# Optimization experiments

Measured on AMD Instinct MI355X. Metric: run time of the kernel, lower is better.

The kernel has to match this reference:

```python
import jax, jax.numpy as jnp
import numpy as np

D = 640          # feature dim (x_dim)
C = 64           # number of classes
N = 1024         # support samples (16 shots/class)
Q = 2048         # query samples
REG = 0.3        # reg_param


def setup_inputs() -> dict:
    key = jax.random.key(0)
    k0, k1, k2, k3, k4 = jax.random.split(key, 5)
    X = jax.random.normal(k0, (N, D), jnp.float32)
    y = (jnp.arange(N) % C).astype(jnp.int32)          # every class populated
    Xq = jax.random.normal(k1, (Q, D), jnp.float32)
    # learnable prior parameters (perturbed from the torch init so grads are nontrivial)
    m = 0.02 * jax.random.normal(k2, (1, D), jnp.float32)
    kappa = jnp.array([0.1], jnp.float32)
    nu = jnp.array([float(D)], jnp.float32)
    triu_diag = 1.0 + 0.05 * jax.random.normal(k3, (D,), jnp.float32)
    triu_lower = jnp.eye(D, dtype=jnp.float32) + 0.05 * jax.random.normal(k4, (D, D), jnp.float32)
    return {"X": X, "y": y, "Xq": Xq, "m": m, "kappa": kappa, "nu": nu,
            "triu_diag": triu_diag, "triu_lower": triu_lower}


def reference(X, y, Xq, m, kappa, nu, triu_diag, triu_lower):
    # strictly-lower-triangular mask: triu(ones, 1).T
    mask = jnp.triu(jnp.ones((D, D), X.dtype), 1).T
    L = jnp.diag(jnp.abs(triu_diag)) + triu_lower * mask          # Cholesky-like factor
    kappa_ = jnp.abs(kappa[0]) + 1e-6
    nu_ = jnp.maximum(nu[0], D - 1 + 1e-6)

    onehot = jax.nn.one_hot(y, C, dtype=X.dtype)                   # [N, C]
    Nc = onehot.sum(0)                                             # [C]
    mean_c = (onehot.T @ X) / Nc[:, None]                          # [C, D]
    # MAP posterior mean per class
    w = Nc / (kappa_ + Nc)
    mu = (1.0 - w)[:, None] * m + w[:, None] * mean_c              # [C, D]

    # per-class second moment: S_c = sum_{y=c} x x^T (segmented X^T X)
    Xc = onehot.T[:, :, None] * X[None, :, :]                      # [C, N, D]
    S = jnp.einsum('cnd,ne->cde', Xc, X)                           # [C, D, D]

    LLt = L @ L.T
    mm = m.T @ m                                                   # [D, D]
    mu_outer = jnp.einsum('cd,ce->cde', mu, mu)
    sigma = (LLt[None] + S + kappa_ * mm[None]
             - (kappa_ + Nc)[:, None, None] * mu_outer)
    sigma = sigma / (nu_ + Nc + D + 2)[:, None, None]
    sigma_inv = jnp.linalg.inv(sigma)
    sigma_inv = (1.0 - REG) * sigma_inv + REG * jnp.eye(D, dtype=X.dtype)

    # batched Mahalanobis quadratic form: -(x - mu_c)^T Sinv_c (x - mu_c)
    diff = Xq[:, None, :] - mu[None, :, :]                         # [Q, C, D]
    dist = jnp.einsum('qcd,cde,qce->qc', diff, sigma_inv, diff)
    return -dist
```

## Files before the change

kernel.cpp:

```cpp
#include <hip/hip_runtime.h>
#include <hip/hip_bf16.h>


#define D 640
#define C 64
#define NSUP 1024
#define Q 2048
#define KMAX 16
#define R18 18
#define VROWS (C * R18)
#define YROWS 3137
#define YPAD 3200
#define NEXT 704
#define LP 40

typedef __attribute__((ext_vector_type(8))) short bf16x8;
typedef __attribute__((ext_vector_type(4))) float floatx4;

__device__ __forceinline__ unsigned short f2bf(float x) {
    unsigned int u = __float_as_uint(x);
    unsigned int r = u + 0x7FFFu + ((u >> 16) & 1u);
    return (unsigned short)(r >> 16);
}

__device__ __forceinline__ void pack4(const float* vv, unsigned short* hp, unsigned short* lp) {
#pragma unroll
    for (int i = 0; i < 4; ++i) {
        unsigned short hb = f2bf(vv[i]);
        float hf = __uint_as_float((unsigned int)hb << 16);
        hp[i] = hb;
        lp[i] = f2bf(vv[i] - hf);
    }
}

__device__ __forceinline__ void rownorm_body(const float* __restrict__ A, int ld,
                                             float* __restrict__ out, int gw, int lane) {
    const float* row = A + (size_t)gw * ld;
    float s = 0.f;
    for (int d = lane; d < D; d += 64) { float v = row[d]; s += v * v; }
#pragma unroll
    for (int off = 32; off; off >>= 1) s += __shfl_xor(s, off);
    if (lane == 0) out[gw] = s;
}

#define BZCH (640 * 640 / 8)
#define AZCH (63 * 640 / 8)
__global__ void k_setup(const int* __restrict__ y, const float* __restrict__ kappa,
                        const float* __restrict__ nu, const float* __restrict__ diag,
                        int* __restrict__ cnt, int* __restrict__ idx,
                        float* __restrict__ sc, float* __restrict__ rd,
                        int* __restrict__ rowmap,
                        unsigned short* __restrict__ Ah, unsigned short* __restrict__ Al,
                        unsigned short* __restrict__ Bh, unsigned short* __restrict__ Bl) {
    int tid = threadIdx.x;
    if (blockIdx.x > 0) {
        int id = (blockIdx.x - 1) * 256 + tid;
        const uint4 z = {0u, 0u, 0u, 0u};
        if (id < BZCH) ((uint4*)Bh)[id] = z;
        else if (id < 2 * BZCH) ((uint4*)Bl)[id - BZCH] = z;
        else if (id < 2 * BZCH + AZCH) ((uint4*)(Ah + (size_t)YROWS * D))[id - 2 * BZCH] = z;
        else if (id < 2 * BZCH + 2 * AZCH) ((uint4*)(Al + (size_t)YROWS * D))[id - 2 * BZCH - AZCH] = z;
        return;
    }
    __shared__ int lc[C];
    if (tid < C) lc[tid] = 0;
    __syncthreads();
    for (int n = tid; n < NSUP; n += 256) {
        int c = y[n];
        int k = atomicAdd(&lc[c], 1);
        if (k < KMAX) idx[c * KMAX + k] = n;
    }
    __syncthreads();
    for (int d = tid; d < D; d += 256) rd[d] = 1.0f / fabsf(diag[d]);
    if (tid < C) {
        int n = lc[tid]; if (n > KMAX) n = KMAX;
        cnt[tid] = n;
        float kap = fabsf(kappa[0]) + 1e-6f;
        float nuv = fmaxf(nu[0], (float)(D - 1) + 1e-6f);
        float Ncf = (float)n;
        sc[64 + tid]  = Ncf / (kap + Ncf);
        sc[128 + tid] = nuv + Ncf + (float)(D + 2);
        sc[192 + tid] = -1.0f / (kap + Ncf);
        if (tid == 0) { sc[0] = kap; sc[1] = nuv; }
    }
    __syncthreads();
    for (int i = tid; i < VROWS; i += 256) {
        int c = i / R18, j = i - c * R18;
        int nc = lc[c] < KMAX ? lc[c] : KMAX;
        int rm;
        if (j == 0) rm = Q + NSUP;
        else if (j <= KMAX) rm = (j - 1 < nc) ? Q + idx[c * KMAX + j - 1] : -1;
        else rm = Q + NSUP + 1 + c;
        rowmap[i] = rm;
    }
}

__global__ __launch_bounds__(256) void k_dinv_mu(
        const float* __restrict__ tlow, const float* __restrict__ rd,
        float* __restrict__ Linv,
        const float* __restrict__ X, const float* __restrict__ m,
        const int* __restrict__ cnt, const int* __restrict__ idx,
        const float* __restrict__ sc, float* __restrict__ mu,
        const float* __restrict__ Xq,
        unsigned short* __restrict__ Ah, unsigned short* __restrict__ Al,
        unsigned short* __restrict__ Bh, unsigned short* __restrict__ Bl,
        float* __restrict__ a0) {
    __shared__ float Lst[128 * 128];
    int tid = threadIdx.x;
    int bid = blockIdx.x;
    if (bid < 160) {
        int b = bid >> 5;
        int j = ((bid & 31) << 2) + (tid >> 6);
        int lane = tid & 63;
        int bB = b * 128;
        {
            float4 tv[16];
            float rv[16];
#pragma unroll
            for (int u = 0; u < 16; ++u) {
                int e = tid + u * 256;
                int c4 = (e & 31) * 4, r = e >> 5;
                tv[u] = *(const float4*)(tlow + (size_t)(bB + r) * D + bB + c4);
                rv[u] = rd[bB + r];
            }
#pragma unroll
            for (int u = 0; u < 16; ++u) {
                int e = tid + u * 256;
                int c4 = (e & 31) * 4, r = e >> 5;
                float vv[4] = {tv[u].x, tv[u].y, tv[u].z, tv[u].w};
#pragma unroll
                for (int t = 0; t < 4; ++t) {
                    int c = c4 + t;
                    float v;
                    if (r == c) v = 1.0f;
                    else if (r > c) v = rv[u] * vv[t];
                    else v = 0.f;
                    Lst[c * 128 + (r ^ (c & 63))] = v;
                }
            }
        }
        __syncthreads();
        float rd0 = rd[bB + lane], rd1 = rd[bB + 64 + lane];
        float acc0 = 0.f, acc1 = 0.f, zz0 = 0.f, zz1 = 0.f;
        for (int i = j; i < 128; ++i) {
            int ri = i >> 6, il = i & 63;
            float av = (ri == 0) ? acc0 : acc1;
            float ai = __shfl(av, il);
            float zi = (i == j) ? __shfl((ri == 0) ? rd0 : rd1, il) : -ai;
            int sw = i & 63;
            float l0 = Lst[i * 128 + (lane ^ sw)];
            float l1 = Lst[i * 128 + 64 + (lane ^ sw)];
            if (lane > i) acc0 += l0 * zi;
            if (64 + lane > i) acc1 += l1 * zi;
            if (lane == i) zz0 = zi;
            if (64 + lane == i) zz1 = zi;
        }
        Linv[(size_t)(bB + lane) * D + bB + j] = zz0;
        Linv[(size_t)(bB + 64 + lane) * D + bB + j] = zz1;
        unsigned short h0 = f2bf(zz0);
        float hf0 = __uint_as_float((unsigned int)h0 << 16);
        Bh[(size_t)(bB + lane) * D + bB + j] = h0;
        Bl[(size_t)(bB + lane) * D + bB + j] = f2bf(zz0 - hf0);
        unsigned short h1 = f2bf(zz1);
        float hf1 = __uint_as_float((unsigned int)h1 << 16);
        Bh[(size_t)(bB + 64 + lane) * D + bB + j] = h1;
        Bl[(size_t)(bB + 64 + lane) * D + bB + j] = f2bf(zz1 - hf1);
    } else if (bid < 320) {
        int u = (bid - 160) * 2 + (tid >> 7);
        int c = u / 5, by = u - c * 5;
        int d = by * 128 + (tid & 127);
        int n = cnt[c];
        float s = 0.f;
        for (int k = 0; k < n; ++k) s += X[(size_t)idx[c * KMAX + k] * D + d];
        float w = sc[64 + c];
        float mean = (n > 0) ? s / (float)n : 0.f;
        float val = (1.f - w) * m[d] + w * mean;
        mu[(size_t)c * D + d] = val;
        unsigned short hb = f2bf(val);
        float hf = __uint_as_float((unsigned int)hb << 16);
        unsigned short lb = f2bf(val - hf);
        Ah[(size_t)(Q + NSUP + 1 + c) * D + d] = hb;
        Al[(size_t)(Q + NSUP + 1 + c) * D + d] = lb;
        Bh[(size_t)(D + c) * D + d] = hb;
        Bl[(size_t)(D + c) * D + d] = lb;
    } else if (bid < 2240) {
        int gid = (bid - 320) * 256 + tid;
        int row = gid / 160, c = (gid - row * 160) * 4;
        float4 v = (row < Q) ? *(const float4*)(Xq + (size_t)row * D + c)
                             : *(const float4*)(X + (size_t)(row - Q) * D + c);
        float vv[4] = {v.x, v.y, v.z, v.w};
        ushort4 h, l;
        pack4(vv, (unsigned short*)&h, (unsigned short*)&l);
        *(ushort4*)(Ah + (size_t)row * D + c) = h;
        *(ushort4*)(Al + (size_t)row * D + c) = l;
    } else if (bid == 2240) {
        if (tid < 160) {
            int c = tid * 4;
            float4 v = *(const float4*)(m + c);
            float vv[4] = {v.x, v.y, v.z, v.w};
            ushort4 h, l;
            pack4(vv, (unsigned short*)&h, (unsigned short*)&l);
            *(ushort4*)(Ah + (size_t)(Q + NSUP) * D + c) = h;
            *(ushort4*)(Al + (size_t)(Q + NSUP) * D + c) = l;
        }
    } else {
        int gw = ((bid - 2241) * 256 + tid) >> 6;
        rownorm_body(Xq, D, a0, gw, tid & 63);
    }
}

__global__ void k_lhat(const float* __restrict__ tlow, const float* __restrict__ Linv,
                       float* __restrict__ Lhat) {
    const int bi_tab[10] = {1, 2, 2, 3, 3, 3, 4, 4, 4, 4};
    const int bk_tab[10] = {0, 0, 1, 0, 1, 2, 0, 1, 2, 3};
    int p = blockIdx.y;
    int bi = bi_tab[p], bk = bk_tab[p];
    int tid = threadIdx.x;
    int c = tid & 127;
    int r = (blockIdx.x << 1) + (tid >> 7);
    const float* drow = Linv + (size_t)(bi * 128 + r) * D + bi * 128;
    const float* lcol = tlow + (size_t)(bi * 128) * D + bk * 128 + c;
    float s = 0.f;
#pragma unroll 4
    for (int t = 0; t < 128; ++t) s += drow[t] * lcol[(size_t)t * D];
    Lhat[(size_t)(bi * 128 + r) * D + bk * 128 + c] = s;
}

template<int B>
__device__ __forceinline__ void linv_chain(const float* __restrict__ Lhat,
                                           float* __restrict__ Linv,
                                           unsigned short* __restrict__ Bh,
                                           unsigned short* __restrict__ Bl,
                                           float S[4][128][20],
                                           int cB, int tid) {
    const int ty = tid >> 2, tx = tid & 3;
    const int r0 = 2 * ty;
    float acc[4 - B][2][4];
#pragma unroll
    for (int a = 0; a < 4 - B; ++a)
#pragma unroll
        for (int rr = 0; rr < 2; ++rr)
#pragma unroll
            for (int cc = 0; cc < 4; ++cc) acc[a][rr][cc] = 0.f;
#pragma unroll
    for (int js = 0; js < 4 - B; ++js) {
        const int j = B + js;
        for (int k0 = 0; k0 < 128; k0 += 8) {
            float svf[8][4];
#pragma unroll
            for (int u = 0; u < 8; ++u) {
                float4 s4 = *(const float4*)&S[js][k0 + u][tx * 4];
                svf[u][0] = s4.x; svf[u][1] = s4.y; svf[u][2] = s4.z; svf[u][3] = s4.w;
            }
#pragma unroll
            for (int a = js; a < 4 - B; ++a) {
                const int i = B + 1 + a;
                const float* p0 = Lhat + (size_t)(i * 128 + r0) * D + j * 128 + k0;
                const float* p1 = p0 + D;
                float4 a00 = *(const float4*)(p0);
                float4 a01 = *(const float4*)(p0 + 4);
                float4 a10 = *(const float4*)(p1);
                float4 a11 = *(const float4*)(p1 + 4);
                float ar0[8] = {a00.x, a00.y, a00.z, a00.w, a01.x, a01.y, a01.z, a01.w};
                float ar1[8] = {a10.x, a10.y, a10.z, a10.w, a11.x, a11.y, a11.z, a11.w};
#pragma unroll
                for (int u = 0; u < 8; ++u) {
#pragma unroll
                    for (int cc = 0; cc < 4; ++cc) {
                        acc[a][0][cc] += ar0[u] * svf[u][cc];
                        acc[a][1][cc] += ar1[u] * svf[u][cc];
                    }
                }
            }
        }
        {
            const int i = j + 1;
#pragma unroll
            for (int rr = 0; rr < 2; ++rr) {
                const int r = r0 + rr;
                float vv[4];
#pragma unroll
                for (int cc = 0; cc < 4; ++cc) vv[cc] = -acc[js][rr][cc];
                float4 v = {vv[0], vv[1], vv[2], vv[3]};
                if (js + 1 < 4 - B) *(float4*)&S[js + 1][r][tx * 4] = v;
                *(float4*)(Linv + (size_t)(i * 128 + r) * D + cB + tx * 4) = v;
                ushort4 hh, ll;
                pack4(vv, (unsigned short*)&hh, (unsigned short*)&ll);
                *(ushort4*)(Bh + (size_t)(i * 128 + r) * D + cB + tx * 4) = hh;
                *(ushort4*)(Bl + (size_t)(i * 128 + r) * D + cB + tx * 4) = ll;
            }
        }
        if (js + 1 < 4 - B) __syncthreads();
    }
}

__global__ __launch_bounds__(256) void k_linv_fill(const float* __restrict__ Lhat,
                                                   float* __restrict__ Linv,
                                                   unsigned short* __restrict__ Bh,
                                                   unsigned short* __restrict__ Bl) {
    __shared__ __align__(16) float S[4][128][20];
    int tid = threadIdx.x;
    int b = blockIdx.x >> 3, strip = blockIdx.x & 7;
    int bB = b * 128, cB = bB + strip * 16;
    {
        int r = tid >> 1, c0 = (tid & 1) * 8;
        const float* src = Linv + (size_t)(bB + r) * D + cB + c0;
        *(float4*)&S[0][r][c0]     = *(const float4*)(src);
        *(float4*)&S[0][r][c0 + 4] = *(const float4*)(src + 4);
    }
    __syncthreads();
    if (b == 0)      linv_chain<0>(Lhat, Linv, Bh, Bl, S, cB, tid);
    else if (b == 1) linv_chain<1>(Lhat, Linv, Bh, Bl, S, cB, tid);
    else if (b == 2) linv_chain<2>(Lhat, Linv, Bh, Bl, S, cB, tid);
    else             linv_chain<3>(Lhat, Linv, Bh, Bl, S, cB, tid);
}

__global__ __launch_bounds__(256) void k_mfma_nt(
        const unsigned short* __restrict__ Ah, const unsigned short* __restrict__ Al,
        const unsigned short* __restrict__ Bh, const unsigned short* __restrict__ Bl,
        float* __restrict__ Out, int M, int N, int ldo,
        unsigned short* __restrict__ Th, unsigned short* __restrict__ Tl) {
    __shared__ __align__(16) unsigned short SB[2][4][64 * LP];
    int tid = threadIdx.x;
    int rowBase = blockIdx.y * 64, colBase = blockIdx.x * 64;
    int r = tid >> 2, e = (tid & 3) << 3;
    int gr = rowBase + r;
    int gc = colBase + r;
    bool aok = (gr < M), bok = (gc < N);
    int w = tid >> 6, lane = tid & 63, q = lane >> 4, lr = lane & 15;
    int aoff = (16 * w + lr) * LP + q * 8;
    int wr = r * LP + e;
    const uint4 z4 = {0u, 0u, 0u, 0u};
    floatx4 acc[4] = {{0.f, 0.f, 0.f, 0.f}, {0.f, 0.f, 0.f, 0.f},
                      {0.f, 0.f, 0.f, 0.f}, {0.f, 0.f, 0.f, 0.f}};
    uint4 vah, val, vbh, vbl;
#define LOADK(kk) { \
        vah = aok ? *(const uint4*)(Ah + (size_t)gr * D + (kk) + e) : z4; \
        val = aok ? *(const uint4*)(Al + (size_t)gr * D + (kk) + e) : z4; \
        vbh = bok ? *(const uint4*)(Bh + (size_t)gc * D + (kk) + e) : z4; \
        vbl = bok ? *(const uint4*)(Bl + (size_t)gc * D + (kk) + e) : z4; }
    LOADK(0);
    for (int step = 0; step < D / 32; ++step) {
        int cur = step & 1;
        *(uint4*)(&SB[cur][0][wr]) = vah;
        *(uint4*)(&SB[cur][1][wr]) = val;
        *(uint4*)(&SB[cur][2][wr]) = vbh;
        *(uint4*)(&SB[cur][3][wr]) = vbl;
        if (step + 1 < D / 32) LOADK((step + 1) * 32);
        __syncthreads();
        bf16x8 ah = *(const bf16x8*)(&SB[cur][0][aoff]);
        bf16x8 al = *(const bf16x8*)(&SB[cur][1][aoff]);
#pragma unroll
        for (int tt = 0; tt < 4; ++tt) {
            int boff = (16 * tt + lr) * LP + q * 8;
            bf16x8 bh = *(const bf16x8*)(&SB[cur][2][boff]);
            bf16x8 bl = *(const bf16x8*)(&SB[cur][3][boff]);
            acc[tt] = __builtin_amdgcn_mfma_f32_16x16x32_bf16(ah, bh, acc[tt], 0, 0, 0);
            acc[tt] = __builtin_amdgcn_mfma_f32_16x16x32_bf16(ah, bl, acc[tt], 0, 0, 0);
            acc[tt] = __builtin_amdgcn_mfma_f32_16x16x32_bf16(al, bh, acc[tt], 0, 0, 0);
        }
    }
#undef LOADK
#pragma unroll
    for (int tt = 0; tt < 4; ++tt) {
        int gc2 = colBase + 16 * tt + lr;
#pragma unroll
        for (int rg = 0; rg < 4; ++rg) {
            int gr2 = rowBase + 16 * w + q * 4 + rg;
            if (gr2 < M && gc2 < N) {
                float v = acc[tt][rg];
                Out[(size_t)gr2 * ldo + gc2] = v;
                if (Th && gc2 < D) {
                    unsigned short hb = f2bf(v);
                    float hf = __uint_as_float((unsigned int)hb << 16);
                    Th[(size_t)gr2 * D + gc2] = hb;
                    Tl[(size_t)gr2 * D + gc2] = f2bf(v - hf);
                }
            }
        }
    }
}

__global__ __launch_bounds__(256) void k_gv(
        const unsigned short* __restrict__ Th, const unsigned short* __restrict__ Tl,
        const int* __restrict__ rowmap, float* __restrict__ G,
        const float* __restrict__ Yt, const float* __restrict__ mu,
        const float* __restrict__ sc, float* __restrict__ at,
        float* __restrict__ h, float* __restrict__ btil,
        float* __restrict__ b0, float* __restrict__ kinv) {
    __shared__ __align__(16) char smem[40960];
    int bid = blockIdx.x, tid = threadIdx.x;
    if (bid < 64) {
        float (*aug)[40] = (float(*)[40])smem;
        int* rmv = (int*)(smem + 2880);
        int c = bid;
        if (tid < R18) rmv[tid] = rowmap[c * R18 + tid];
        for (int i2 = tid; i2 < R18 * R18; i2 += 256)
            aug[i2 / R18][R18 + i2 % R18] = (i2 / R18 == i2 % R18) ? 1.f : 0.f;
        __syncthreads();
        if (tid < 171) {
            int i = 0, rem = tid;
            while (rem >= R18 - i) { rem -= R18 - i; ++i; }
            int j = i + rem;
            int rmi = rmv[i], rmj = rmv[j];
            float s = 0.f;
            if (rmi >= 0 && rmj >= 0) {
                const float* ri = Yt + (size_t)rmi * NEXT;
                const float* rj = Yt + (size_t)rmj * NEXT;
                float s0 = 0.f, s1 = 0.f, s2 = 0.f, s3 = 0.f;
#pragma unroll 4
                for (int d = 0; d < D; d += 4) {
                    float4 a = *(const float4*)(ri + d);
                    float4 bb = *(const float4*)(rj + d);
                    s0 += a.x * bb.x; s1 += a.y * bb.y;
                    s2 += a.z * bb.z; s3 += a.w * bb.w;
                }
                s = (s0 + s1) + (s2 + s3);
            }
            aug[i][j] = s;
            if (i != j) aug[j][i] = s;
        }
        __syncthreads();
        int w = tid >> 6, lane = tid & 63;
        if (w == 1) {
            const float* mc = mu + (size_t)c * D;
            float s = 0.f;
            for (int d = lane; d < D; d += 64) { float v = mc[d]; s += v * v; }
#pragma unroll
            for (int off = 32; off; off >>= 1) s += __shfl_xor(s, off);
            if (lane == 0) b0[c] = s;
        }
        if (w == 0) {
            if (lane < R18) h[c * R18 + lane] = aug[lane][R18 - 1];
            if (lane == 0) btil[c] = aug[R18 - 1][R18 - 1];
            volatile float (*va)[40] = (volatile float (*)[40])aug;
            if (lane == 0) va[0][0] += 1.0f / sc[0];
            else if (lane <= KMAX) va[lane][lane] += 1.0f;
            else if (lane == R18 - 1) va[R18 - 1][R18 - 1] += sc[192 + c];
            __threadfence_block();
            for (int p = 0; p < R18; ++p) {
                float v = (lane >= p && lane < R18) ? fabsf(va[lane][p]) : -1.f;
                int bi = lane;
#pragma unroll
                for (int off = 32; off; off >>= 1) {
                    float ov = __shfl_xor(v, off);
                    int oi = __shfl_xor(bi, off);
                    if (ov > v || (ov == v && oi < bi)) { v = ov; bi = oi; }
                }
                float pv = va[bi][p];
                if (lane < 2 * R18) {
                    float rp = va[bi][lane];
                    if (bi != p) va[bi][lane] = va[p][lane];
                    va[p][lane] = rp / pv;
                }
                __threadfence_block();
                float f  = (lane < R18) ? va[lane][p] : 0.f;
                float pr = (lane < 2 * R18) ? va[p][lane] : 0.f;
#pragma unroll
                for (int it = 0; it < 11; ++it) {
                    int e = lane + it * 64;
                    int r2 = e / 36, cc = e - r2 * 36;
                    float fr = __shfl(f, r2 < R18 ? r2 : 0);
                    float pc = __shfl(pr, cc);
                    if (e < R18 * 2 * R18 && r2 != p) va[r2][cc] -= fr * pc;
                }
                __threadfence_block();
            }
            for (int e = lane; e < R18 * R18; e += 64)
                kinv[(size_t)c * R18 * R18 + e] = va[e / R18][R18 + e % R18];
        }
    } else if (bid < 640) {
        unsigned short (*SB)[4][64 * LP] = (unsigned short (*)[4][64 * LP])smem;
        int gb = bid - 64;
        int rowBase = (gb / 18) * 64, colBase = (gb % 18) * 64;
        int r = tid >> 2, e = (tid & 3) << 3;
        int gr = rowBase + r;
        int gc = colBase + r;
        int br = rowmap[gc];
        int w = tid >> 6, lane = tid & 63, q = lane >> 4, lr = lane & 15;
        int aoff = (16 * w + lr) * LP + q * 8;
        int wr = r * LP + e;
        const uint4 z4 = {0u, 0u, 0u, 0u};
        floatx4 acc[4] = {{0.f, 0.f, 0.f, 0.f}, {0.f, 0.f, 0.f, 0.f},
                          {0.f, 0.f, 0.f, 0.f}, {0.f, 0.f, 0.f, 0.f}};
        uint4 vah, val, vbh, vbl;
#define LOADG(kk) { \
            vah = *(const uint4*)(Th + (size_t)gr * D + (kk) + e); \
            val = *(const uint4*)(Tl + (size_t)gr * D + (kk) + e); \
            vbh = (br >= 0) ? *(const uint4*)(Th + (size_t)br * D + (kk) + e) : z4; \
            vbl = (br >= 0) ? *(const uint4*)(Tl + (size_t)br * D + (kk) + e) : z4; }
        LOADG(0);
        for (int step = 0; step < D / 32; ++step) {
            int cur = step & 1;
            *(uint4*)(&SB[cur][0][wr]) = vah;
            *(uint4*)(&SB[cur][1][wr]) = val;
            *(uint4*)(&SB[cur][2][wr]) = vbh;
            *(uint4*)(&SB[cur][3][wr]) = vbl;
            if (step + 1 < D / 32) LOADG((step + 1) * 32);
            __syncthreads();
            bf16x8 ah = *(const bf16x8*)(&SB[cur][0][aoff]);
            bf16x8 al = *(const bf16x8*)(&SB[cur][1][aoff]);
#pragma unroll
            for (int tt = 0; tt < 4; ++tt) {
                int boff = (16 * tt + lr) * LP + q * 8;
                bf16x8 bh = *(const bf16x8*)(&SB[cur][2][boff]);
                bf16x8 bl = *(const bf16x8*)(&SB[cur][3][boff]);
                acc[tt] = __builtin_amdgcn_mfma_f32_16x16x32_bf16(ah, bh, acc[tt], 0, 0, 0);
                acc[tt] = __builtin_amdgcn_mfma_f32_16x16x32_bf16(ah, bl, acc[tt], 0, 0, 0);
                acc[tt] = __builtin_amdgcn_mfma_f32_16x16x32_bf16(al, bh, acc[tt], 0, 0, 0);
            }
        }
#undef LOADG
#pragma unroll
        for (int tt = 0; tt < 4; ++tt) {
            int gc2 = colBase + 16 * tt + lr;
#pragma unroll
            for (int rg = 0; rg < 4; ++rg) {
                int gr2 = rowBase + 16 * w + q * 4 + rg;
                G[(size_t)gr2 * VROWS + gc2] = acc[tt][rg];
            }
        }
    } else {
        int gw = ((bid - 640) * 256 + tid) >> 6;
        rownorm_body(Yt, NEXT, at, gw, tid & 63);
    }
}

__global__ void k_epi(const float* __restrict__ G, const float* __restrict__ Yt,
                      const float* __restrict__ at, const float* __restrict__ a0,
                      const float* __restrict__ h, const float* __restrict__ btil,
                      const float* __restrict__ b0, const float* __restrict__ kinv,
                      const float* __restrict__ sc, float* __restrict__ out) {
    __shared__ float lk[R18 * R18], lh[R18];
    __shared__ float ldn, lbt, lb0;
    int c = blockIdx.x, tid = threadIdx.x;
    for (int i = tid; i < R18 * R18; i += 256) lk[i] = kinv[(size_t)c * R18 * R18 + i];
    if (tid < R18) lh[tid] = h[c * R18 + tid];
    if (tid == 0) { ldn = sc[128 + c]; lbt = btil[c]; lb0 = b0[c]; }
    __syncthreads();
    int q = blockIdx.y * 256 + tid;
    const float* Gr = G + (size_t)q * VROWS + c * R18;
    float g[R18];
#pragma unroll
    for (int j = 0; j < R18; ++j) g[j] = Gr[j];
    float ipt = g[R18 - 1];
#pragma unroll
    for (int j = 0; j < R18; ++j) g[j] -= lh[j];
    float corr = 0.f;
#pragma unroll
    for (int i = 0; i < R18; ++i) {
        float s = 0.f;
#pragma unroll
        for (int j = 0; j < R18; ++j) s += lk[i * R18 + j] * g[j];
        corr += g[i] * s;
    }
    float ip0 = Yt[(size_t)q * NEXT + D + c];
    float tt = at[q] - 2.f * ipt + lbt;
    float t0 = a0[q] - 2.f * ip0 + lb0;
    out[(size_t)q * C + c] = -(0.7f * ldn * (tt - corr) + 0.3f * t0);
}

extern "C" void kernel_launch(void* const* d_in, const int* in_sizes, int n_in,
                              void* d_out, int out_size, void* d_ws, size_t ws_size,
                              hipStream_t stream) {
    const float* X     = (const float*)d_in[0];
    const int*   y     = (const int*)d_in[1];
    const float* Xq    = (const float*)d_in[2];
    const float* m     = (const float*)d_in[3];
    const float* kappa = (const float*)d_in[4];
    const float* nu    = (const float*)d_in[5];
    const float* tdiag = (const float*)d_in[6];
    const float* tlow  = (const float*)d_in[7];
    float* out = (float*)d_out;

    char* w = (char*)d_ws;
    auto alloc = [&](size_t bytes) {
        char* p = w;
        w += (bytes + 255) & ~(size_t)255;
        return p;
    };
    int*   cnt    = (int*)alloc(C * 4);
    int*   idx    = (int*)alloc(C * KMAX * 4);
    int*   rowmap = (int*)alloc(VROWS * 4);
    float* sc     = (float*)alloc(256 * 4);
    float* rd     = (float*)alloc(D * 4);
    float* mu     = (float*)alloc((size_t)C * D * 4);
    float* at     = (float*)alloc(Q * 4);
    float* a0     = (float*)alloc(Q * 4);
    float* h      = (float*)alloc(C * R18 * 4);
    float* btil   = (float*)alloc(C * 4);
    float* b0     = (float*)alloc(C * 4);
    float* kinv   = (float*)alloc((size_t)C * R18 * R18 * 4);
    float* Ytout  = (float*)alloc((size_t)YPAD * NEXT * 4);
    unsigned short* Th = (unsigned short*)alloc((size_t)YPAD * D * 2);
    unsigned short* Tl = (unsigned short*)alloc((size_t)YPAD * D * 2);
    unsigned short* Bh = (unsigned short*)alloc((size_t)NEXT * D * 2);
    unsigned short* Bl = (unsigned short*)alloc((size_t)NEXT * D * 2);
    char* wmark = w;
    float* Linv = (float*)alloc((size_t)D * D * 4);
    float* Lhat = (float*)alloc((size_t)D * D * 4);
    unsigned short* Ah = (unsigned short*)alloc((size_t)YPAD * D * 2);
    unsigned short* Al = (unsigned short*)alloc((size_t)YPAD * D * 2);
    w = wmark;
    float* G    = (float*)alloc((size_t)Q * VROWS * 4);

    k_setup<<<441, 256, 0, stream>>>(y, kappa, nu, tdiag, cnt, idx, sc, rd, rowmap,
                                     Ah, Al, Bh, Bl);
    k_dinv_mu<<<2753, 256, 0, stream>>>(tlow, rd, Linv, X, m, cnt, idx, sc, mu,
                                        Xq, Ah, Al, Bh, Bl, a0);
    k_lhat<<<dim3(64, 10), 256, 0, stream>>>(tlow, Linv, Lhat);
    k_linv_fill<<<32, 256, 0, stream>>>(Lhat, Linv, Bh, Bl);
    k_mfma_nt<<<dim3(NEXT / 64, YPAD / 64), 256, 0, stream>>>(
        Ah, Al, Bh, Bl, Ytout, YPAD, NEXT, NEXT, Th, Tl);
    k_gv<<<1152, 256, 0, stream>>>(Th, Tl, rowmap, G, Ytout, mu, sc, at,
                                   h, btil, b0, kinv);
    k_epi<<<dim3(C, Q / 256), 256, 0, stream>>>(G, Ytout, at, a0, h, btil, b0, kinv, sc, out);
}
```

Before: 227.3 us.

## Remap GEMM workgroups per XCD, drop LDS padding, stage Gram rows in LDS

Adds an XCD-aware workgroup remapping so that consecutive tiles land on the same XCD and share L2, applied to both the generic MFMA GEMM and the G-matrix blocks. Removes the LDS row padding (LP 40 → 32), which shrinks shared memory but can add bank conflicts on the bf16x8 reads. In the per-class Gram/inverse blocks, the 18 gathered Y rows are first loaded cooperatively into LDS, so the 171 dot-product threads no longer each re-read global memory. This raises the shared memory request of k_gv, which may lower occupancy.

```diff
diff --git a/kernel.cpp b/kernel.cpp
--- a/kernel.cpp
+++ b/kernel.cpp
@@ -12,7 +12,6 @@
 #define YROWS 3137
 #define YPAD 3200
 #define NEXT 704
-#define LP 40
 
 typedef __attribute__((ext_vector_type(8))) short bf16x8;
 typedef __attribute__((ext_vector_type(4))) float floatx4;
@@ -41,6 +40,13 @@
 #pragma unroll
     for (int off = 32; off; off >>= 1) s += __shfl_xor(s, off);
     if (lane == 0) out[gw] = s;
+}
+
+__device__ __forceinline__ int xcd_chunk(int orig, int nwg) {
+    int q = nwg >> 3, r = nwg & 7;
+    int xcd = orig & 7, pos = orig >> 3;
+    return (xcd < r) ? xcd * (q + 1) + pos
+                     : r * (q + 1) + (xcd - r) * q + pos;
 }
 
 #define BZCH (640 * 640 / 8)
@@ -320,16 +326,19 @@
         const unsigned short* __restrict__ Bh, const unsigned short* __restrict__ Bl,
         float* __restrict__ Out, int M, int N, int ldo,
         unsigned short* __restrict__ Th, unsigned short* __restrict__ Tl) {
-    __shared__ __align__(16) unsigned short SB[2][4][64 * LP];
+    __shared__ unsigned short SB[2][4][64 * 32];
     int tid = threadIdx.x;
-    int rowBase = blockIdx.y * 64, colBase = blockIdx.x * 64;
+    int nbx = gridDim.x, nwg = nbx * gridDim.y;
+    int orig = blockIdx.y * nbx + blockIdx.x;
+    int wgid = xcd_chunk(orig, nwg);
+    int rowBase = (wgid / nbx) * 64, colBase = (wgid % nbx) * 64;
     int r = tid >> 2, e = (tid & 3) << 3;
     int gr = rowBase + r;
     int gc = colBase + r;
     bool aok = (gr < M), bok = (gc < N);
     int w = tid >> 6, lane = tid & 63, q = lane >> 4, lr = lane & 15;
-    int aoff = (16 * w + lr) * LP + q * 8;
-    int wr = r * LP + e;
+    int aoff = (16 * w + lr) * 32 + q * 8;
+    int wr = r * 32 + e;
     const uint4 z4 = {0u, 0u, 0u, 0u};
     floatx4 acc[4] = {{0.f, 0.f, 0.f, 0.f}, {0.f, 0.f, 0.f, 0.f},
                       {0.f, 0.f, 0.f, 0.f}, {0.f, 0.f, 0.f, 0.f}};
@@ -352,7 +361,7 @@
         bf16x8 al = *(const bf16x8*)(&SB[cur][1][aoff]);
 #pragma unroll
         for (int tt = 0; tt < 4; ++tt) {
-            int boff = (16 * tt + lr) * LP + q * 8;
+            int boff = (16 * tt + lr) * 32 + q * 8;
             bf16x8 bh = *(const bf16x8*)(&SB[cur][2][boff]);
             bf16x8 bl = *(const bf16x8*)(&SB[cur][3][boff]);
             acc[tt] = __builtin_amdgcn_mfma_f32_16x16x32_bf16(ah, bh, acc[tt], 0, 0, 0);
@@ -388,38 +397,61 @@
         const float* __restrict__ sc, float* __restrict__ at,
         float* __restrict__ h, float* __restrict__ btil,
         float* __restrict__ b0, float* __restrict__ kinv) {
-    __shared__ __align__(16) char smem[40960];
+    __shared__ __align__(16) char smem[49344];
     int bid = blockIdx.x, tid = threadIdx.x;
     if (bid < 64) {
-        float (*aug)[40] = (float(*)[40])smem;
-        int* rmv = (int*)(smem + 2880);
+        float (*sv)[644] = (float(*)[644])smem;
+        float (*aug)[40] = (float(*)[40])(smem + 46368);
+        int* rmv = (int*)(smem + 46368 + 2880);
         int c = bid;
         if (tid < R18) rmv[tid] = rowmap[c * R18 + tid];
-        for (int i2 = tid; i2 < R18 * R18; i2 += 256)
-            aug[i2 / R18][R18 + i2 % R18] = (i2 / R18 == i2 % R18) ? 1.f : 0.f;
+        __syncthreads();
+        {
+            int rmu[12];
+#pragma unroll
+            for (int u = 0; u < 12; ++u) {
+                int i = tid + u * 256;
+                int r = i / 160;
+                rmu[u] = (i < R18 * 160) ? rmv[r] : -1;
+            }
+            float4 buf[12];
+            const float4 z = {0.f, 0.f, 0.f, 0.f};
+#pragma unroll
+            for (int u = 0; u < 12; ++u) {
+                int i = tid + u * 256;
+                int d4 = (i - (i / 160) * 160) * 4;
+                buf[u] = (rmu[u] >= 0) ? *(const float4*)(Yt + (size_t)rmu[u] * NEXT + d4) : z;
+            }
+#pragma unroll
+            for (int u = 0; u < 12; ++u) {
+                int i = tid + u * 256;
+                if (i < R18 * 160) {
+                    int r = i / 160, d4 = (i - r * 160) * 4;
+                    *(float4*)&sv[r][d4] = buf[u];
+                }
+            }
+        }
         __syncthreads();
         if (tid < 171) {
             int i = 0, rem = tid;
             while (rem >= R18 - i) { rem -= R18 - i; ++i; }
             int j = i + rem;
-            int rmi = rmv[i], rmj = rmv[j];
-            float s = 0.f;
-            if (rmi >= 0 && rmj >= 0) {
-                const float* ri = Yt + (size_t)rmi * NEXT;
-                const float* rj = Yt + (size_t)rmj * NEXT;
-                float s0 = 0.f, s1 = 0.f, s2 = 0.f, s3 = 0.f;
+            const float* ri = sv[i];
+            const float* rj = sv[j];
+            float s0 = 0.f, s1 = 0.f, s2 = 0.f, s3 = 0.f;
 #pragma unroll 4
-                for (int d = 0; d < D; d += 4) {
-                    float4 a = *(const float4*)(ri + d);
-                    float4 bb = *(const float4*)(rj + d);
-                    s0 += a.x * bb.x; s1 += a.y * bb.y;
-                    s2 += a.z * bb.z; s3 += a.w * bb.w;
-                }
-                s = (s0 + s1) + (s2 + s3);
-            }
+            for (int d = 0; d < D; d += 4) {
+                float4 a = *(const float4*)(ri + d);
+                float4 bb = *(const float4*)(rj + d);
+                s0 += a.x * bb.x; s1 += a.y * bb.y;
+                s2 += a.z * bb.z; s3 += a.w * bb.w;
+            }
+            float s = (s0 + s1) + (s2 + s3);
             aug[i][j] = s;
             if (i != j) aug[j][i] = s;
         }
+        for (int i2 = tid; i2 < R18 * R18; i2 += 256)
+            aug[i2 / R18][R18 + i2 % R18] = (i2 / R18 == i2 % R18) ? 1.f : 0.f;
         __syncthreads();
         int w = tid >> 6, lane = tid & 63;
         if (w == 1) {
@@ -470,16 +502,17 @@
                 kinv[(size_t)c * R18 * R18 + e] = va[e / R18][R18 + e % R18];
         }
     } else if (bid < 640) {
-        unsigned short (*SB)[4][64 * LP] = (unsigned short (*)[4][64 * LP])smem;
-        int gb = bid - 64;
+        unsigned short (*SB)[4][64 * 32] = (unsigned short (*)[4][64 * 32])smem;
+        int gb0 = bid - 64;
+        int gb = xcd_chunk(gb0, 576);
         int rowBase = (gb / 18) * 64, colBase = (gb % 18) * 64;
         int r = tid >> 2, e = (tid & 3) << 3;
         int gr = rowBase + r;
         int gc = colBase + r;
         int br = rowmap[gc];
         int w = tid >> 6, lane = tid & 63, q = lane >> 4, lr = lane & 15;
-        int aoff = (16 * w + lr) * LP + q * 8;
-        int wr = r * LP + e;
+        int aoff = (16 * w + lr) * 32 + q * 8;
+        int wr = r * 32 + e;
         const uint4 z4 = {0u, 0u, 0u, 0u};
         floatx4 acc[4] = {{0.f, 0.f, 0.f, 0.f}, {0.f, 0.f, 0.f, 0.f},
                           {0.f, 0.f, 0.f, 0.f}, {0.f, 0.f, 0.f, 0.f}};
@@ -502,7 +535,7 @@
             bf16x8 al = *(const bf16x8*)(&SB[cur][1][aoff]);
 #pragma unroll
             for (int tt = 0; tt < 4; ++tt) {
-                int boff = (16 * tt + lr) * LP + q * 8;
+                int boff = (16 * tt + lr) * 32 + q * 8;
                 bf16x8 bh = *(const bf16x8*)(&SB[cur][2][boff]);
                 bf16x8 bl = *(const bf16x8*)(&SB[cur][3][boff]);
                 acc[tt] = __builtin_amdgcn_mfma_f32_16x16x32_bf16(ah, bh, acc[tt], 0, 0, 0);
```

After: 212.1 us. 6.7% less time.
